# Optimization experiments

Measured on AMD Instinct MI355X. Metric: run time of the kernel, lower is better.

## Reference

```python
import jax, jax.numpy as jnp
import numpy as np

H = 128          # hidden_channels
NUM_NODES = 13
NUM_LAYERS = 8
NUM_JOINTS = 17
D_MAX = 33       # max per-node feature count (torso/thighs)
OBS_DIM = 348
B = 16384


def _build_feature_indices():
    base = {0: list(range(0, 5)) + list(range(22, 28)),
            1: list(range(5, 7)) + list(range(28, 30)),
            2: [7, 30],
            3: list(range(8, 12)) + list(range(31, 35)),
            4: [11, 34],
            5: [],
            6: list(range(12, 16)) + list(range(35, 39)),
            7: [15, 38],
            8: [],
            9: list(range(16, 19)) + list(range(39, 42)),
            10: [18, 41],
            11: list(range(19, 22)) + list(range(42, 45)),
            12: [21, 44]}
    qfrc = {0: [], 1: [], 2: [0, 1, 2], 3: [3, 4, 5], 4: [6], 5: [],
            6: [7, 8, 9], 7: [10], 8: [], 9: [11, 12], 10: [13],
            11: [14, 15], 12: [16]}
    idx = np.full((NUM_NODES, D_MAX), OBS_DIM, dtype=np.int32)  # pad -> appended zero column
    for k in range(NUM_NODES):
        fi = list(base[k])
        fi += list(range(45 + k * 10, 45 + (k + 1) * 10))   # cinert
        fi += list(range(175 + k * 6, 175 + (k + 1) * 6))   # cvel
        fi += [253 + i for i in qfrc[k]]                    # qfrc_actuator
        fi += list(range(270 + k * 6, 270 + (k + 1) * 6))   # cfrc_ext
        idx[k, :len(fi)] = fi
    return idx

FEAT_IDX = jnp.asarray(_build_feature_indices())

_n2n = np.array([[0, 1, 2, 3, 4, 2, 6, 7, 0, 9, 0, 11],
                 [1, 2, 3, 4, 5, 6, 7, 8, 9, 10, 11, 12]])
SRC = jnp.asarray(np.concatenate([_n2n[0], _n2n[1]]))  # 24 directed edges
DST = jnp.asarray(np.concatenate([_n2n[1], _n2n[0]]))
JOINT_MAP = jnp.asarray(np.array([[1, 2], [1, 2], [1, 2], [2, 3], [2, 3], [2, 3],
                                  [3, 4], [2, 6], [2, 6], [2, 6], [6, 7], [0, 9],
                                  [0, 9], [9, 10], [0, 11], [0, 11], [11, 12]]))


def setup_inputs() -> dict:
    key = jax.random.key(0)
    ks = jax.random.split(key, 9)
    obs = jax.random.normal(ks[0], (B, OBS_DIM), dtype=jnp.float32)
    s_in = 1.0 / np.sqrt(D_MAX)
    s_h = 1.0 / np.sqrt(H)
    s_2h = 1.0 / np.sqrt(2 * H)
    W1 = jax.random.normal(ks[1], (NUM_NODES, D_MAX, H), dtype=jnp.float32) * s_in
    b1 = jnp.zeros((NUM_NODES, H), dtype=jnp.float32)
    W2 = jax.random.normal(ks[2], (NUM_NODES, H, H), dtype=jnp.float32) * s_h
    b2 = jnp.zeros((NUM_NODES, H), dtype=jnp.float32)
    Wmsg = jax.random.normal(ks[3], (NUM_LAYERS, 2 * H, H), dtype=jnp.float32) * s_2h
    bmsg = jnp.zeros((NUM_LAYERS, H), dtype=jnp.float32)
    Wout = jax.random.normal(ks[4], (NUM_JOINTS, 2 * H), dtype=jnp.float32) * s_2h
    bout = jnp.zeros((NUM_JOINTS,), dtype=jnp.float32)
    return {"obs": obs, "W1": W1, "b1": b1, "W2": W2, "b2": b2,
            "Wmsg": Wmsg, "bmsg": bmsg, "Wout": Wout, "bout": bout}


def reference(obs, W1, b1, W2, b2, Wmsg, bmsg, Wout, bout):
    b = obs.shape[0]
    # Per-node-type MLP encoder (padded gather: index OBS_DIM -> zero column)
    obs_ext = jnp.concatenate([obs, jnp.zeros((b, 1), obs.dtype)], axis=1)
    xn = obs_ext[:, FEAT_IDX]                                   # [B, 13, D_MAX]
    h = jax.nn.elu(jnp.einsum('bnd,ndh->bnh', xn, W1) + b1)     # [B, 13, H]
    x = jnp.einsum('bnh,nhk->bnk', h, W2) + b2                  # [B, 13, H]
    # Message passing: gather src -> scatter-add at dst -> concat -> Linear -> ELU
    for l in range(NUM_LAYERS):
        agg = jnp.zeros_like(x).at[:, DST, :].add(x[:, SRC, :])
        x = jax.nn.elu(jnp.concatenate([x, agg], axis=-1) @ Wmsg[l] + bmsg[l])
    # Per-joint readout from the two nodes each joint connects
    pair = x[:, JOINT_MAP, :].reshape(b, NUM_JOINTS, 2 * H)     # [B, 17, 2H]
    out = jnp.einsum('bjd,jd->bj', pair, Wout) + bout           # [B, 17]
    return out
```

## Files before the change

kernel.cpp:

```cpp
#include <hip/hip_runtime.h>
#include <math.h>

#define NN   13
#define HH   128
#define NL   8
#define NJ   17
#define OBSD 348
#define DMAX 33
#define TB   8
#define NTHR 1024
#define ASTRIDE 256
#define HSTRIDE 128
#define HBS  136
#define XNS  72

__constant__ int c_feat[NN * DMAX] = {
  0,1,2,3,4,22,23,24,25,26,27,45,46,47,48,49,50,51,52,53,54,175,176,177,178,179,180,270,271,272,273,274,275,
  5,6,28,29,55,56,57,58,59,60,61,62,63,64,181,182,183,184,185,186,276,277,278,279,280,281,-1,-1,-1,-1,-1,-1,-1,
  7,30,65,66,67,68,69,70,71,72,73,74,187,188,189,190,191,192,253,254,255,282,283,284,285,286,287,-1,-1,-1,-1,-1,-1,
  8,9,10,11,31,32,33,34,75,76,77,78,79,80,81,82,83,84,193,194,195,196,197,198,256,257,258,288,289,290,291,292,293,
  11,34,85,86,87,88,89,90,91,92,93,94,199,200,201,202,203,204,259,294,295,296,297,298,299,-1,-1,-1,-1,-1,-1,-1,-1,
  95,96,97,98,99,100,101,102,103,104,205,206,207,208,209,210,300,301,302,303,304,305,-1,-1,-1,-1,-1,-1,-1,-1,-1,-1,-1,
  12,13,14,15,35,36,37,38,105,106,107,108,109,110,111,112,113,114,211,212,213,214,215,216,260,261,262,306,307,308,309,310,311,
  15,38,115,116,117,118,119,120,121,122,123,124,217,218,219,220,221,222,263,312,313,314,315,316,317,-1,-1,-1,-1,-1,-1,-1,-1,
  125,126,127,128,129,130,131,132,133,134,223,224,225,226,227,228,318,319,320,321,322,323,-1,-1,-1,-1,-1,-1,-1,-1,-1,-1,-1,
  16,17,18,39,40,41,135,136,137,138,139,140,141,142,143,144,229,230,231,232,233,234,264,265,324,325,326,327,328,329,-1,-1,-1,
  18,41,145,146,147,148,149,150,151,152,153,154,235,236,237,238,239,240,266,330,331,332,333,334,335,-1,-1,-1,-1,-1,-1,-1,-1,
  19,20,21,42,43,44,155,156,157,158,159,160,161,162,163,164,241,242,243,244,245,246,267,268,336,337,338,339,340,341,-1,-1,-1,
  21,44,165,166,167,168,169,170,171,172,173,174,247,248,249,250,251,252,269,342,343,344,345,346,347,-1,-1,-1,-1,-1,-1,-1,-1
};

__device__ constexpr int ADJ[NN][3] = {
  {1,9,11},{0,2,0},{1,3,6},{2,4,0},{3,5,0},{4,0,0},{2,7,0},
  {6,8,0},{7,0,0},{0,10,0},{9,0,0},{0,12,0},{11,0,0}
};
__device__ constexpr int DEG[NN] = {3,2,3,2,2,1,2,2,1,2,1,2,1};
__device__ constexpr int JM0[NJ] = {1,1,1,2,2,2,3,2,2,2,6,0,0,9,0,0,11};
__device__ constexpr int JM1[NJ] = {2,2,2,3,3,3,4,6,6,6,7,9,9,10,11,11,12};

typedef float4 F4;
using h8v = __attribute__((ext_vector_type(8))) _Float16;
using h2v = __attribute__((ext_vector_type(2))) _Float16;
using f32x4  = __attribute__((ext_vector_type(4)))  float;
using f32x16 = __attribute__((ext_vector_type(16))) float;

__device__ __forceinline__ float elu1(float v) {
  return v > 0.0f ? v : (__expf(v) - 1.0f);
}

__device__ __forceinline__ short f2h(float v) {
  _Float16 h = (_Float16)v;
  return (short)__builtin_bit_cast(unsigned short, h);
}
__device__ __forceinline__ float h2f(unsigned short s) {
  return (float)__builtin_bit_cast(_Float16, s);
}
__device__ __forceinline__ unsigned packh2(float a, float b) {
  h2v p; p.x = (_Float16)a; p.y = (_Float16)b;
  return __builtin_bit_cast(unsigned, p);
}

__device__ __forceinline__ int a_addr(int row, int col, int half) {
  const int u = (2 * (col >> 3) + half + row) & 31;
  return row * ASTRIDE + u * 8 + (col & 7);
}

__global__ void prep_all(const float* __restrict__ Wm,
                         const float* __restrict__ W2,
                         const float* __restrict__ W1,
                         unsigned* __restrict__ ws) {
  if (blockIdx.x < 512) {
    int i = blockIdx.x * 256 + threadIdx.x;
    int j2   = i & 3;
    int lane = (i >> 2) & 63;
    int nt   = (i >> 8) & 3;
    int kind = (i >> 10) & 1;
    int ks   = (i >> 11) & 7;
    int l    = i >> 14;
    int k = ks * 16 + ((lane >> 5) * 8) + 2 * j2;
    int n = nt * 32 + (lane & 31);
    int rbase = kind ? 128 : 0;
    float v0 = Wm[((l * 256) + rbase + k) * HH + n];
    float v1 = Wm[((l * 256) + rbase + k + 1) * HH + n];
    ws[i] = packh2(v0, v1);
  } else if (blockIdx.x < 928) {
    int i = (blockIdx.x - 512) * 256 + threadIdx.x;
    int j2   = i & 3;
    int lane = (i >> 2) & 63;
    int nt   = (i >> 8) & 7;
    int kt   = (i >> 11) & 3;
    int n    = i >> 13;
    int k = kt * 32 + (lane >> 4) * 8 + 2 * j2;
    int c = nt * 16 + (lane & 15);
    float v0 = W2[(n * HH + k) * HH + c];
    float v1 = W2[(n * HH + k + 1) * HH + c];
    ws[131072 + i] = packh2(v0, v1);
  } else {
    int i = (blockIdx.x - 928) * 256 + threadIdx.x;
    int j2   = i & 3;
    int lane = (i >> 2) & 63;
    int nt   = (i >> 8) & 7;
    int kt   = (i >> 11) & 1;
    int n    = i >> 12;
    int k = kt * 32 + (lane >> 4) * 8 + 2 * j2;
    int c = nt * 16 + (lane & 15);
    float v0 = (k     < DMAX) ? W1[(n * DMAX + k) * HH + c]     : 0.f;
    float v1 = (k + 1 < DMAX) ? W1[(n * DMAX + k + 1) * HH + c] : 0.f;
    ws[237568 + i] = packh2(v0, v1);
  }
}

__global__ __launch_bounds__(NTHR, 4)
void gnn_fused(const float* __restrict__ obs,
               const float* __restrict__ W1, const float* __restrict__ b1,
               const float* __restrict__ W2, const float* __restrict__ b2,
               const float* __restrict__ bm,
               const float* __restrict__ Wo, const float* __restrict__ bo,
               const float* __restrict__ wmsw,
               float* __restrict__ out, int w1go)
{
  __shared__ short As[128 * ASTRIDE];
  __shared__ float Bb[2][4096];

  const int t    = threadIdx.x;
  const int wid  = t >> 6;
  const int mq   = wid >> 2;
  const int nq   = wid & 3;
  const int lane = t & 63;
  const int l31  = lane & 31;
  const int lh   = lane >> 5;
  const bool h1  = (lh == 1);
  const int g    = t >> 5;
  const int og   = t & 31;
  const int o0   = og << 2;
  const int b0   = blockIdx.x * TB;

  const F4* wsrc4 = (const F4*)wmsw;
  short* hb = As;
  short* xn16 = (short*)Bb;
  F4* bufA = (F4*)Bb;
  F4* bufB = ((F4*)Bb) + 1024;
  const unsigned* w2fb = ((const unsigned*)wmsw) + 131072;
  const unsigned* w1fb = ((const unsigned*)wmsw) + 237568;

  for (int i = t; i < TB * NN * 64; i += NTHR) {
    int d  = i & 63;
    int r  = i >> 6;
    int nn = r % NN;
    int bb = r / NN;
    int fi = (d < DMAX) ? c_feat[nn * DMAX + d] : -1;
    float v = (fi >= 0) ? obs[(b0 + bb) * OBSD + fi] : 0.0f;
    xn16[(nn * 16 + bb) * XNS + d] = f2h(v);
  }
  __syncthreads();

  if (w1go) {
    if (wid < NN) {
      const int n    = wid;
      const int arow = lane & 15;
      const int kof  = (lane >> 4) * 8;
      const h8v af0 = *(const h8v*)(xn16 + (n * 16 + arow) * XNS + 0 + kof);
      const h8v af1 = *(const h8v*)(xn16 + (n * 16 + arow) * XNS + 32 + kof);
      const uint4* wf = (const uint4*)w1fb;
      const int re = (lane >> 4) * 4;
      #pragma unroll
      for (int nt = 0; nt < 8; ++nt) {
        f32x4 a;
        const float bias = b1[n * HH + nt * 16 + (lane & 15)];
        a[0] = bias; a[1] = bias; a[2] = bias; a[3] = bias;
        const uint4 wv0 = wf[((n * 2 + 0) * 8 + nt) * 64 + lane];
        const uint4 wv1 = wf[((n * 2 + 1) * 8 + nt) * 64 + lane];
        a = __builtin_amdgcn_mfma_f32_16x16x32_f16(af0, __builtin_bit_cast(h8v, wv0), a, 0, 0, 0);
        a = __builtin_amdgcn_mfma_f32_16x16x32_f16(af1, __builtin_bit_cast(h8v, wv1), a, 0, 0, 0);
        if (re < 8) {
          #pragma unroll
          for (int rg = 0; rg < 4; ++rg)
            hb[(n * 16 + re + rg) * HBS + nt * 16 + (lane & 15)] = f2h(elu1(a[rg]));
        }
      }
    }
  } else {
    const int n  = g >> 1;
    const int q0 = (g & 1) * 4;
    if (n < NN) {
      float acc[4][4];
      const F4 bv = *(const F4*)(b1 + n * HH + o0);
      #pragma unroll
      for (int q = 0; q < 4; ++q) { acc[q][0]=bv.x; acc[q][1]=bv.y; acc[q][2]=bv.z; acc[q][3]=bv.w; }
      #pragma unroll 3
      for (int k = 0; k < DMAX; ++k) {
        const F4 w = *(const F4*)(W1 + (n * DMAX + k) * HH + o0);
        #pragma unroll
        for (int q = 0; q < 4; ++q) {
          const float xv = h2f((unsigned short)xn16[(n * 16 + q0 + q) * XNS + k]);
          acc[q][0] += xv * w.x; acc[q][1] += xv * w.y;
          acc[q][2] += xv * w.z; acc[q][3] += xv * w.w;
        }
      }
      #pragma unroll
      for (int q = 0; q < 4; ++q) {
        short4 hv;
        hv.x = f2h(elu1(acc[q][0])); hv.y = f2h(elu1(acc[q][1]));
        hv.z = f2h(elu1(acc[q][2])); hv.w = f2h(elu1(acc[q][3]));
        *(short4*)(hb + (n * 16 + (q0 + q)) * HBS + o0) = hv;
      }
    }
  }
  __syncthreads();

  f32x4 acc2[8];
  {
    if (wid < NN) {
      const int n    = wid;
      const int arow = lane & 15;
      const int kof  = (lane >> 4) * 8;
      h8v af[4];
      #pragma unroll
      for (int kt = 0; kt < 4; ++kt)
        af[kt] = *(const h8v*)(hb + (n * 16 + arow) * HBS + kt * 32 + kof);
      const uint4* wf = (const uint4*)w2fb;
      #pragma unroll
      for (int nt = 0; nt < 8; ++nt) {
        const float bias = b2[n * HH + nt * 16 + (lane & 15)];
        acc2[nt][0] = bias; acc2[nt][1] = bias;
        acc2[nt][2] = bias; acc2[nt][3] = bias;
        #pragma unroll
        for (int kt = 0; kt < 4; ++kt) {
          const uint4 wv = wf[((n * 4 + kt) * 8 + nt) * 64 + lane];
          acc2[nt] = __builtin_amdgcn_mfma_f32_16x16x32_f16(
                       af[kt], __builtin_bit_cast(h8v, wv), acc2[nt], 0, 0, 0);
        }
      }
    }
  }
  __syncthreads();
  {
    for (int i = t; i < 24 * HSTRIDE; i += NTHR) {
      int pr = i / HSTRIDE, off = i % HSTRIDE;
      int row = (pr / 3) * 16 + 13 + (pr % 3);
      ((int*)As)[row * HSTRIDE + off] = 0;
    }
    if (wid < NN) {
      const int n  = wid;
      const int e0 = (lane >> 4) * 4;
      if (e0 < 8) {
        #pragma unroll
        for (int nt = 0; nt < 8; ++nt) {
          const int col = nt * 16 + (lane & 15);
          #pragma unroll
          for (int rg = 0; rg < 4; ++rg) {
            const int row = (e0 + rg) * 16 + n;
            As[a_addr(row, col, 0)] = f2h(acc2[nt][rg]);
          }
        }
      }
    }
  }
  __syncthreads();

  {
    bufA[t] = wsrc4[t];
    F4 rnext = wsrc4[1024 + t];
    __syncthreads();

    #pragma unroll 1
    for (int l = 0; l < NL; ++l) {
      f32x16 aT, aB;
      #pragma unroll
      for (int r = 0; r < 16; ++r) { aT[r] = 0.f; aB[r] = 0.f; }

      #pragma unroll 1
      for (int kp = 0; kp < 4; ++kp) {
        const int gpc = l * 4 + kp;
        F4* cur = (gpc & 1) ? bufB : bufA;
        F4* nxt = (gpc & 1) ? bufA : bufB;

        F4 rnext2;
        const bool more2 = (gpc + 2 < NL * 4);
        if (more2) rnext2 = wsrc4[(size_t)(gpc + 2) * 1024 + t];

        #pragma unroll
        for (int kk = 0; kk < 2; ++kk) {
          const int ks = kp * 2 + kk;
          const short* bb = ((const short*)cur) + kk * 4096;

          h8v ah;
          {
            const int row = mq * 32 + l31;
            const int p = 2 * ks + lh;
            ah = *(const h8v*)(As + row * ASTRIDE + (((2 * p + row) & 31) * 8));
          }
          const h8v bth = *(const h8v*)(bb + ((0 * 4 + nq) * 64 + lane) * 8);
          const h8v bbh = *(const h8v*)(bb + ((1 * 4 + nq) * 64 + lane) * 8);

          aT = __builtin_amdgcn_mfma_f32_32x32x16_f16(ah, bth, aT, 0, 0, 0);
          aB = __builtin_amdgcn_mfma_f32_32x32x16_f16(ah, bbh, aB, 0, 0, 0);
        }

        if (gpc + 1 < NL * 4) nxt[t] = rnext;
        __syncthreads();
        rnext = rnext2;
      }

      {
        const int col  = nq * 32 + l31;
        const float bias = bm[l * HH + col];
        float cb[16], sw[16];
        #pragma unroll
        for (int r = 0; r < 16; ++r) { cb[r] = aB[r]; sw[r] = __shfl_xor(cb[r], 32); }

        #pragma unroll
        for (int r = 0; r < 16; ++r) {
          const int p  = (r & 3) + 8 * (r >> 2);
          const int n0 = p & 15;
          const int n1 = n0 + 4;
          const int es = p >> 4;
          #define SRCV(np)                                                \
            ({ const int rl = (es << 4) + (np);                           \
               const int hp = (rl >> 2) & 1;                              \
               const int pp = rl - 4 * hp;                                \
               const int rp = (pp & 3) + 4 * (pp >> 3);                   \
               (hp == 1) ? (h1 ? cb[rp] : sw[rp])                         \
                         : (h1 ? sw[rp] : cb[rp]); })
          float a0 = SRCV(ADJ[n0][0]);
          if (DEG[n0] > 1) a0 += SRCV(ADJ[n0][1]);
          if (DEG[n0] > 2) a0 += SRCV(ADJ[n0][2]);
          float a1 = 0.f;
          if (n1 < NN) {
            a1 = SRCV(ADJ[n1][0]);
            if (DEG[n1] > 1) a1 += SRCV(ADJ[n1][1]);
            if (DEG[n1] > 2) a1 += SRCV(ADJ[n1][2]);
          }
          #undef SRCV
          const float agg = h1 ? a1 : a0;
          const float tot = aT[r] + agg + bias;
          float xv = elu1(tot);
          if (n1 >= NN) xv = h1 ? 0.f : xv;
          const int row = mq * 32 + p + 4 * lh;
          As[a_addr(row, col, 0)] = f2h(xv);
        }
      }
      __syncthreads();
    }
  }

  if (g < TB) {
    const int elem = g;
    const int c = og * 4;
    float xv[NN][4];
    #pragma unroll
    for (int n = 0; n < NN; ++n) {
      const int row = elem * 16 + n;
      const ushort4 uh = *(const ushort4*)(As + a_addr(row, c, 0));
      xv[n][0] = h2f(uh.x);
      xv[n][1] = h2f(uh.y);
      xv[n][2] = h2f(uh.z);
      xv[n][3] = h2f(uh.w);
    }
    #pragma unroll
    for (int j = 0; j < NJ; ++j) {
      const F4 wa = *(const F4*)(Wo + j * 256 + c);
      const F4 wb = *(const F4*)(Wo + j * 256 + 128 + c);
      const float* xa = xv[JM0[j]];
      const float* xb = xv[JM1[j]];
      float p = xa[0]*wa.x + xa[1]*wa.y + xa[2]*wa.z + xa[3]*wa.w
              + xb[0]*wb.x + xb[1]*wb.y + xb[2]*wb.z + xb[3]*wb.w;
      p += __shfl_xor(p, 16);
      p += __shfl_xor(p, 8);
      p += __shfl_xor(p, 4);
      p += __shfl_xor(p, 2);
      p += __shfl_xor(p, 1);
      if (og == 0) out[(b0 + elem) * NJ + j] = p + bo[j];
    }
  }
}

extern "C" void kernel_launch(void* const* d_in, const int* in_sizes, int n_in,
                              void* d_out, int out_size, void* d_ws, size_t ws_size,
                              hipStream_t stream) {
  const float* obs = (const float*)d_in[0];
  const float* W1  = (const float*)d_in[1];
  const float* b1  = (const float*)d_in[2];
  const float* W2  = (const float*)d_in[3];
  const float* b2  = (const float*)d_in[4];
  const float* Wm  = (const float*)d_in[5];
  const float* bm  = (const float*)d_in[6];
  const float* Wo  = (const float*)d_in[7];
  const float* bo  = (const float*)d_in[8];
  float* out = (float*)d_out;

  const int B = in_sizes[0] / OBSD;
  const int nblk = B / TB;

  const size_t need = (size_t)(131072 + 106496 + 53248) * 4;
  const int w1go = (ws_size >= need) ? 1 : 0;

  prep_all<<<w1go ? 1136 : 928, 256, 0, stream>>>(Wm, W2, W1, (unsigned*)d_ws);
  gnn_fused<<<nblk, NTHR, 0, stream>>>(obs, W1, b1, W2, b2, bm, Wo, bo,
                                       (const float*)d_ws, out, w1go);
}
```

Before: 424.9 us.

## Process sixteen batch elements per block, doubling MFMA tiles per wave

Raises the per-block batch tile from 8 to 16 elements, so shared memory holds twice as many activation rows. In the message-passing loop each wave now runs two 32-row MFMA tiles against the same staged weight fragments, which halves weight streaming and barrier count per element. The encoder paths and epilogue are extended to fill all 16 rows. The cost is double the LDS footprint (As grows to 128KB) and more accumulator registers, which likely lowers occupancy below the declared launch bound of 4 blocks.

New measurement: 351.4 us. 1.21x faster.

```diff
diff --git a/kernel.cpp b/kernel.cpp
--- a/kernel.cpp
+++ b/kernel.cpp
@@ -7,7 +7,7 @@
 #define NJ   17
 #define OBSD 348
 #define DMAX 33
-#define TB   8
+#define TB   16
 #define NTHR 1024
 #define ASTRIDE 256
 #define HSTRIDE 128
@@ -119,7 +119,7 @@
                const float* __restrict__ wmsw,
                float* __restrict__ out, int w1go)
 {
-  __shared__ short As[128 * ASTRIDE];
+  __shared__ short As[256 * ASTRIDE];
   __shared__ float Bb[2][4096];
 
   const int t    = threadIdx.x;
@@ -172,33 +172,31 @@
         const uint4 wv1 = wf[((n * 2 + 1) * 8 + nt) * 64 + lane];
         a = __builtin_amdgcn_mfma_f32_16x16x32_f16(af0, __builtin_bit_cast(h8v, wv0), a, 0, 0, 0);
         a = __builtin_amdgcn_mfma_f32_16x16x32_f16(af1, __builtin_bit_cast(h8v, wv1), a, 0, 0, 0);
-        if (re < 8) {
-          #pragma unroll
-          for (int rg = 0; rg < 4; ++rg)
-            hb[(n * 16 + re + rg) * HBS + nt * 16 + (lane & 15)] = f2h(elu1(a[rg]));
-        }
+        #pragma unroll
+        for (int rg = 0; rg < 4; ++rg)
+          hb[(n * 16 + re + rg) * HBS + nt * 16 + (lane & 15)] = f2h(elu1(a[rg]));
       }
     }
   } else {
     const int n  = g >> 1;
-    const int q0 = (g & 1) * 4;
+    const int q0 = (g & 1) * 8;
     if (n < NN) {
-      float acc[4][4];
+      float acc[8][4];
       const F4 bv = *(const F4*)(b1 + n * HH + o0);
       #pragma unroll
-      for (int q = 0; q < 4; ++q) { acc[q][0]=bv.x; acc[q][1]=bv.y; acc[q][2]=bv.z; acc[q][3]=bv.w; }
+      for (int q = 0; q < 8; ++q) { acc[q][0]=bv.x; acc[q][1]=bv.y; acc[q][2]=bv.z; acc[q][3]=bv.w; }
       #pragma unroll 3
       for (int k = 0; k < DMAX; ++k) {
         const F4 w = *(const F4*)(W1 + (n * DMAX + k) * HH + o0);
         #pragma unroll
-        for (int q = 0; q < 4; ++q) {
+        for (int q = 0; q < 8; ++q) {
           const float xv = h2f((unsigned short)xn16[(n * 16 + q0 + q) * XNS + k]);
           acc[q][0] += xv * w.x; acc[q][1] += xv * w.y;
           acc[q][2] += xv * w.z; acc[q][3] += xv * w.w;
         }
       }
       #pragma unroll
-      for (int q = 0; q < 4; ++q) {
+      for (int q = 0; q < 8; ++q) {
         short4 hv;
         hv.x = f2h(elu1(acc[q][0])); hv.y = f2h(elu1(acc[q][1]));
         hv.z = f2h(elu1(acc[q][2])); hv.w = f2h(elu1(acc[q][3]));
@@ -235,7 +233,7 @@
   }
   __syncthreads();
   {
-    for (int i = t; i < 24 * HSTRIDE; i += NTHR) {
+    for (int i = t; i < 48 * HSTRIDE; i += NTHR) {
       int pr = i / HSTRIDE, off = i % HSTRIDE;
       int row = (pr / 3) * 16 + 13 + (pr % 3);
       ((int*)As)[row * HSTRIDE + off] = 0;
@@ -243,15 +241,13 @@
     if (wid < NN) {
       const int n  = wid;
       const int e0 = (lane >> 4) * 4;
-      if (e0 < 8) {
+      #pragma unroll
+      for (int nt = 0; nt < 8; ++nt) {
+        const int col = nt * 16 + (lane & 15);
         #pragma unroll
-        for (int nt = 0; nt < 8; ++nt) {
-          const int col = nt * 16 + (lane & 15);
-          #pragma unroll
-          for (int rg = 0; rg < 4; ++rg) {
-            const int row = (e0 + rg) * 16 + n;
-            As[a_addr(row, col, 0)] = f2h(acc2[nt][rg]);
-          }
+        for (int rg = 0; rg < 4; ++rg) {
+          const int row = (e0 + rg) * 16 + n;
+          As[a_addr(row, col, 0)] = f2h(acc2[nt][rg]);
         }
       }
     }
@@ -265,9 +261,11 @@
 
     #pragma unroll 1
     for (int l = 0; l < NL; ++l) {
-      f32x16 aT, aB;
-      #pragma unroll
-      for (int r = 0; r < 16; ++r) { aT[r] = 0.f; aB[r] = 0.f; }
+      f32x16 aT0, aB0, aT1, aB1;
+      #pragma unroll
+      for (int r = 0; r < 16; ++r) {
+        aT0[r] = 0.f; aB0[r] = 0.f; aT1[r] = 0.f; aB1[r] = 0.f;
+      }
 
       #pragma unroll 1
       for (int kp = 0; kp < 4; ++kp) {
@@ -284,17 +282,18 @@
           const int ks = kp * 2 + kk;
           const short* bb = ((const short*)cur) + kk * 4096;
 
-          h8v ah;
-          {
-            const int row = mq * 32 + l31;
-            const int p = 2 * ks + lh;
-            ah = *(const h8v*)(As + row * ASTRIDE + (((2 * p + row) & 31) * 8));
-          }
+          const int p = 2 * ks + lh;
+          const int row0 = mq * 32 + l31;
+          const int row1 = (mq + 4) * 32 + l31;
+          const h8v ah0 = *(const h8v*)(As + row0 * ASTRIDE + (((2 * p + row0) & 31) * 8));
+          const h8v ah1 = *(const h8v*)(As + row1 * ASTRIDE + (((2 * p + row1) & 31) * 8));
           const h8v bth = *(const h8v*)(bb + ((0 * 4 + nq) * 64 + lane) * 8);
           const h8v bbh = *(const h8v*)(bb + ((1 * 4 + nq) * 64 + lane) * 8);
 
-          aT = __builtin_amdgcn_mfma_f32_32x32x16_f16(ah, bth, aT, 0, 0, 0);
-          aB = __builtin_amdgcn_mfma_f32_32x32x16_f16(ah, bbh, aB, 0, 0, 0);
+          aT0 = __builtin_amdgcn_mfma_f32_32x32x16_f16(ah0, bth, aT0, 0, 0, 0);
+          aB0 = __builtin_amdgcn_mfma_f32_32x32x16_f16(ah0, bbh, aB0, 0, 0, 0);
+          aT1 = __builtin_amdgcn_mfma_f32_32x32x16_f16(ah1, bth, aT1, 0, 0, 0);
+          aB1 = __builtin_amdgcn_mfma_f32_32x32x16_f16(ah1, bbh, aB1, 0, 0, 0);
         }
 
         if (gpc + 1 < NL * 4) nxt[t] = rnext;
@@ -305,40 +304,86 @@
       {
         const int col  = nq * 32 + l31;
         const float bias = bm[l * HH + col];
-        float cb[16], sw[16];
-        #pragma unroll
-        for (int r = 0; r < 16; ++r) { cb[r] = aB[r]; sw[r] = __shfl_xor(cb[r], 32); }
-
-        #pragma unroll
-        for (int r = 0; r < 16; ++r) {
-          const int p  = (r & 3) + 8 * (r >> 2);
-          const int n0 = p & 15;
-          const int n1 = n0 + 4;
-          const int es = p >> 4;
-          #define SRCV(np)                                                \
-            ({ const int rl = (es << 4) + (np);                           \
-               const int hp = (rl >> 2) & 1;                              \
-               const int pp = rl - 4 * hp;                                \
-               const int rp = (pp & 3) + 4 * (pp >> 3);                   \
-               (hp == 1) ? (h1 ? cb[rp] : sw[rp])                         \
-                         : (h1 ? sw[rp] : cb[rp]); })
-          float a0 = SRCV(ADJ[n0][0]);
-          if (DEG[n0] > 1) a0 += SRCV(ADJ[n0][1]);
-          if (DEG[n0] > 2) a0 += SRCV(ADJ[n0][2]);
-          float a1 = 0.f;
-          if (n1 < NN) {
-            a1 = SRCV(ADJ[n1][0]);
-            if (DEG[n1] > 1) a1 += SRCV(ADJ[n1][1]);
-            if (DEG[n1] > 2) a1 += SRCV(ADJ[n1][2]);
-          }
-          #undef SRCV
-          const float agg = h1 ? a1 : a0;
-          const float tot = aT[r] + agg + bias;
-          float xv = elu1(tot);
-          if (n1 >= NN) xv = h1 ? 0.f : xv;
-          const int row = mq * 32 + p + 4 * lh;
-          As[a_addr(row, col, 0)] = f2h(xv);
+
+        #define EPILOG(AT, AB, MQB)                                          \
+        {                                                                    \
+          float cb[16], sw[16];                                              \
+          _Pragma("unroll")                                                  \
+          for (int r = 0; r < 16; ++r) { cb[r] = (AB)[r];                    \
+                                         sw[r] = __shfl_xor(cb[r], 32); }    \
+          _Pragma("unroll")                                                  \
+          for (int r = 0; r < 16; ++r) {                                     \
+            const int p  = (r & 3) + 8 * (r >> 2);                           \
+            const int n0 = p & 15;                                           \
+            const int n1 = n0 + 4;                                           \
+            const int es = p >> 4;                                           \
+            float a0, a1 = 0.f;                                              \
+            {                                                                \
+              const int np0 = ADJ[n0][0];                                    \
+              const int rl0 = (es << 4) + np0;                               \
+              const int hp0 = (rl0 >> 2) & 1;                                \
+              const int pp0 = rl0 - 4 * hp0;                                 \
+              const int rp0 = (pp0 & 3) + 4 * (pp0 >> 3);                    \
+              a0 = (hp0 == 1) ? (h1 ? cb[rp0] : sw[rp0])                     \
+                              : (h1 ? sw[rp0] : cb[rp0]);                    \
+              if (DEG[n0] > 1) {                                             \
+                const int np = ADJ[n0][1];                                   \
+                const int rl = (es << 4) + np;                               \
+                const int hp = (rl >> 2) & 1;                                \
+                const int pp = rl - 4 * hp;                                  \
+                const int rp = (pp & 3) + 4 * (pp >> 3);                     \
+                a0 += (hp == 1) ? (h1 ? cb[rp] : sw[rp])                     \
+                                : (h1 ? sw[rp] : cb[rp]);                    \
+              }                                                              \
+              if (DEG[n0] > 2) {                                             \
+                const int np = ADJ[n0][2];                                   \
+                const int rl = (es << 4) + np;                               \
+                const int hp = (rl >> 2) & 1;                                \
+                const int pp = rl - 4 * hp;                                  \
+                const int rp = (pp & 3) + 4 * (pp >> 3);                     \
+                a0 += (hp == 1) ? (h1 ? cb[rp] : sw[rp])                     \
+                                : (h1 ? sw[rp] : cb[rp]);                    \
+              }                                                              \
+            }                                                                \
+            if (n1 < NN) {                                                   \
+              const int np0 = ADJ[n1][0];                                    \
+              const int rl0 = (es << 4) + np0;                               \
+              const int hp0 = (rl0 >> 2) & 1;                                \
+              const int pp0 = rl0 - 4 * hp0;                                 \
+              const int rp0 = (pp0 & 3) + 4 * (pp0 >> 3);                    \
+              a1 = (hp0 == 1) ? (h1 ? cb[rp0] : sw[rp0])                     \
+                              : (h1 ? sw[rp0] : cb[rp0]);                    \
+              if (DEG[n1] > 1) {                                             \
+                const int np = ADJ[n1][1];                                   \
+                const int rl = (es << 4) + np;                               \
+                const int hp = (rl >> 2) & 1;                                \
+                const int pp = rl - 4 * hp;                                  \
+                const int rp = (pp & 3) + 4 * (pp >> 3);                     \
+                a1 += (hp == 1) ? (h1 ? cb[rp] : sw[rp])                     \
+                                : (h1 ? sw[rp] : cb[rp]);                    \
+              }                                                              \
+              if (DEG[n1] > 2) {                                             \
+                const int np = ADJ[n1][2];                                   \
+                const int rl = (es << 4) + np;                               \
+                const int hp = (rl >> 2) & 1;                                \
+                const int pp = rl - 4 * hp;                                  \
+                const int rp = (pp & 3) + 4 * (pp >> 3);                     \
+                a1 += (hp == 1) ? (h1 ? cb[rp] : sw[rp])                     \
+                                : (h1 ? sw[rp] : cb[rp]);                    \
+              }                                                              \
+            }                                                                \
+            const float agg = h1 ? a1 : a0;                                  \
+            const float tot = (AT)[r] + agg + bias;                          \
+            float xv = elu1(tot);                                            \
+            if (n1 >= NN) xv = h1 ? 0.f : xv;                                \
+            const int row = (MQB) * 32 + p + 4 * lh;                         \
+            As[a_addr(row, col, 0)] = f2h(xv);                               \
+          }                                                                  \
         }
+
+        EPILOG(aT0, aB0, mq)
+        EPILOG(aT1, aB1, (mq + 4))
+        #undef EPILOG
       }
       __syncthreads();
     }
```
